# Performance work log

Measured on AMD Instinct MI355X. Metric: run time of the kernel, lower is better.

Reference implementation:

```python
import jax, jax.numpy as jnp
import numpy as np

B, S, H = 2, 2048, 1024
NUM_HEADS = 16
HEAD_DIM = H // NUM_HEADS  # 64
SCALE = HEAD_DIM ** -0.5


def apply_rope(x, cos, sin):
    # x: [B, nh, S, hd]; cos/sin: [1, 1, S, hd//2]
    x1 = x[..., ::2]
    x2 = x[..., 1::2]
    rotated = jnp.stack([x1 * cos - x2 * sin, x1 * sin + x2 * cos], axis=-1)
    return rotated.reshape(x.shape)


def setup_inputs() -> dict:
    key = jax.random.key(0)
    ks = jax.random.split(key, 7)
    return {
        "x": jax.random.normal(ks[0], (B, S, H), dtype=jnp.float32),
        "cos": jax.random.normal(ks[1], (S, HEAD_DIM // 2), dtype=jnp.float32),
        "sin": jax.random.normal(ks[2], (S, HEAD_DIM // 2), dtype=jnp.float32),
        "wq": jax.random.normal(ks[3], (H, H), dtype=jnp.float32) * (H ** -0.5),
        "wk": jax.random.normal(ks[4], (H, H), dtype=jnp.float32) * (H ** -0.5),
        "wv": jax.random.normal(ks[5], (H, H), dtype=jnp.float32) * (H ** -0.5),
        "wo": jax.random.normal(ks[6], (H, H), dtype=jnp.float32) * (H ** -0.5),
    }


def reference(x, cos, sin, wq, wk, wv, wo):
    b, s, h = x.shape
    nh, hd = NUM_HEADS, HEAD_DIM
    # torch Linear: y = x @ W.T
    q = (x @ wq.T).reshape(b, s, nh, hd).transpose(0, 2, 1, 3)  # [b, nh, s, hd]
    k = (x @ wk.T).reshape(b, s, nh, hd).transpose(0, 2, 1, 3)
    v = (x @ wv.T).reshape(b, s, nh, hd).transpose(0, 2, 1, 3)

    c = cos[None, None]  # [1,1,s,hd//2]
    sn = sin[None, None]
    q = apply_rope(q, c, sn)
    k = apply_rope(k, c, sn)

    scores = jnp.einsum("bhqd,bhkd->bhqk", q, k) * SCALE  # [b, nh, s, s]
    causal_mask = jnp.triu(jnp.ones((s, s), dtype=bool), k=1)
    scores = jnp.where(causal_mask[None, None], -jnp.inf, scores)
    attn = jax.nn.softmax(scores, axis=-1)
    out = jnp.einsum("bhqk,bhkd->bhqd", attn, v)  # [b, nh, s, hd]
    out = out.transpose(0, 2, 1, 3).reshape(b, s, h)
    return out @ wo.T
```

## Files before the change

### kernel.cpp

```cpp
#include <hip/hip_runtime.h>

typedef __attribute__((ext_vector_type(8))) __bf16 bf16x8;
typedef __attribute__((ext_vector_type(4))) float f32x4;
typedef __attribute__((ext_vector_type(4))) unsigned short ushort4v;

__device__ __forceinline__ unsigned short f2bf(float x) {
  union { float f; unsigned u; } v; v.f = x;
  unsigned r = v.u + 0x7fffu + ((v.u >> 16) & 1u);
  return (unsigned short)(r >> 16);
}

#define GLDS16(g, l) __builtin_amdgcn_global_load_lds( \
    (__attribute__((address_space(1))) void*)(g), \
    (__attribute__((address_space(3))) void*)(l), 16, 0, 0)

__global__ void cvt_f32_bf16(const float* __restrict__ src,
                             unsigned short* __restrict__ dst, int n4) {
  int i = blockIdx.x * blockDim.x + threadIdx.x;
  if (i >= n4) return;
  float4 v = reinterpret_cast<const float4*>(src)[i];
  ushort4v o;
  o.x = f2bf(v.x); o.y = f2bf(v.y); o.z = f2bf(v.z); o.w = f2bf(v.w);
  reinterpret_cast<ushort4v*>(dst)[i] = o;
}

template <int MODE>
__global__ __launch_bounds__(256) void gemm_bt(
    const unsigned short* __restrict__ A, const unsigned short* __restrict__ Bw,
    const float* __restrict__ cosT, const float* __restrict__ sinT,
    unsigned short* __restrict__ Qh, unsigned short* __restrict__ Kh,
    unsigned short* __restrict__ Vt, float* __restrict__ outF) {
  __shared__ __align__(16) unsigned char smA[2][8192];
  __shared__ __align__(16) unsigned char smB[2][8192];
  const int t = threadIdx.x;
  const int lane = t & 63, wvi = t >> 6;
  const int wr = wvi >> 1, wc = wvi & 1;
  const int g = lane >> 4, li = lane & 15;
  const int row0 = blockIdx.y * 128, col0 = blockIdx.x * 128;

  const int schunk = (t & 3) ^ ((t >> 2) & 3);
  const size_t arow = (size_t)(row0 + (t >> 2)) * 1024 + schunk * 8;
  const size_t brow = (size_t)(col0 + (t >> 2)) * 1024 + schunk * 8;

  f32x4 acc[4][4];
#pragma unroll
  for (int mi = 0; mi < 4; ++mi)
#pragma unroll
    for (int ni = 0; ni < 4; ++ni) acc[mi][ni] = (f32x4){0.f, 0.f, 0.f, 0.f};

  auto stage = [&](int buf, int k0) {
    GLDS16(A + arow + k0, &smA[buf][t * 16]);
    GLDS16(A + arow + 64 * 1024 + k0, &smA[buf][4096 + t * 16]);
    GLDS16(Bw + brow + k0, &smB[buf][t * 16]);
    GLDS16(Bw + brow + 64 * 1024 + k0, &smB[buf][4096 + t * 16]);
  };

  stage(0, 0);
  for (int kk = 0; kk < 32; ++kk) {
    __syncthreads();
    const int buf = kk & 1;
    if (kk < 31) stage(buf ^ 1, (kk + 1) * 32);
    bf16x8 af[4], bfr[4];
#pragma unroll
    for (int mi = 0; mi < 4; ++mi)
      af[mi] = *reinterpret_cast<const bf16x8*>(
          &smA[buf][((wr * 64 + mi * 16 + li) << 6) + ((g ^ (li & 3)) << 4)]);
#pragma unroll
    for (int ni = 0; ni < 4; ++ni)
      bfr[ni] = *reinterpret_cast<const bf16x8*>(
          &smB[buf][((wc * 64 + ni * 16 + li) << 6) + ((g ^ (li & 3)) << 4)]);
#pragma unroll
    for (int mi = 0; mi < 4; ++mi)
#pragma unroll
      for (int ni = 0; ni < 4; ++ni)
        acc[mi][ni] = __builtin_amdgcn_mfma_f32_16x16x32_bf16(
            af[mi], bfr[ni], acc[mi][ni], 0, 0, 0);
  }

#pragma unroll
  for (int mi = 0; mi < 4; ++mi) {
    const int rowb = row0 + wr * 64 + mi * 16 + g * 4;
#pragma unroll
    for (int ni = 0; ni < 4; ++ni) {
      const int col = col0 + wc * 64 + ni * 16 + li;
#pragma unroll
      for (int r = 0; r < 4; ++r) {
        float v = acc[mi][ni][r];
        const int rr = rowb + r;
        if (MODE == 1) {
          outF[(size_t)rr * 1024 + col] = v;
        } else {
          const int s = rr & 2047, b = rr >> 11;
          const int jj = col & 1023;
          const int h = jj >> 6, d = jj & 63;
          const int bh = b * 16 + h;
          const int typ = col >> 10;
          if (typ == 2) {
            Vt[((size_t)bh * 64 + d) * 2048 + s] = f2bf(v);
          } else {
            const float cs = cosT[s * 32 + (d >> 1)];
            const float sn = sinT[s * 32 + (d >> 1)];
            const float pr = __shfl_xor(v, 1);
            float rv = (d & 1) ? (pr * sn + v * cs) : (v * cs - pr * sn);
            if (typ == 0) rv *= 0.18033688011112042f;
            unsigned short* dst = (typ == 0) ? Qh : Kh;
            dst[((size_t)bh * 2048 + s) * 64 + d] = f2bf(rv);
          }
        }
      }
    }
  }
}

__global__ __launch_bounds__(512, 4) void attn_fwd(
    const unsigned short* __restrict__ Qh, const unsigned short* __restrict__ Kh,
    const unsigned short* __restrict__ Vt, unsigned short* __restrict__ Ob) {
  __shared__ __align__(16) unsigned short Plds[2][8][16][72];

  const int t = threadIdx.x, lane = t & 63, w = t >> 6;
  const int wg = w >> 2, wl = w & 3;
  const int g = lane >> 4, li = lane & 15;
  const int bh = blockIdx.x, y = blockIdx.y;
  const int qt = wg ? (31 - y) : y;
  const int q0 = qt * 64;

  const unsigned short* __restrict__ Kbh = Kh + (size_t)bh * 2048 * 64;
  const unsigned short* __restrict__ Vbh = Vt + (size_t)bh * 64 * 2048;

  bf16x8 qa[2];
  {
    const unsigned short* qrow =
        Qh + ((size_t)bh * 2048 + q0 + wl * 16 + li) * 64 + g * 8;
    qa[0] = *reinterpret_cast<const bf16x8*>(qrow);
    qa[1] = *reinterpret_cast<const bf16x8*>(qrow + 32);
  }

  float m_[4], l_[4];
  f32x4 oacc[4];
#pragma unroll
  for (int r = 0; r < 4; ++r) { m_[r] = -1e30f; l_[r] = 0.f; }
#pragma unroll
  for (int dt = 0; dt < 4; ++dt) oacc[dt] = (f32x4){0.f, 0.f, 0.f, 0.f};

  for (int kt = 0; kt <= qt; ++kt) {
    const int kv0 = kt * 64;
    const int par = kt & 1;

    f32x4 sacc[4];
#pragma unroll
    for (int ct = 0; ct < 4; ++ct) {
      const unsigned short* krow = Kbh + (size_t)(kv0 + ct * 16 + li) * 64 + g * 8;
      bf16x8 kb0 = *reinterpret_cast<const bf16x8*>(krow);
      bf16x8 kb1 = *reinterpret_cast<const bf16x8*>(krow + 32);
      f32x4 z = (f32x4){0.f, 0.f, 0.f, 0.f};
      z = __builtin_amdgcn_mfma_f32_16x16x32_bf16(qa[0], kb0, z, 0, 0, 0);
      z = __builtin_amdgcn_mfma_f32_16x16x32_bf16(qa[1], kb1, z, 0, 0, 0);
      sacc[ct] = z;
    }

    bf16x8 vb[8];
#pragma unroll
    for (int dt = 0; dt < 4; ++dt) {
      const unsigned short* vrow = Vbh + (size_t)(dt * 16 + li) * 2048 + kv0 + g * 8;
      vb[2 * dt] = *reinterpret_cast<const bf16x8*>(vrow);
      vb[2 * dt + 1] = *reinterpret_cast<const bf16x8*>(vrow + 32);
    }

    if (kt == qt) {
#pragma unroll
      for (int ct = 0; ct < 4; ++ct)
#pragma unroll
        for (int r = 0; r < 4; ++r)
          if (ct * 16 + li > wl * 16 + g * 4 + r) sacc[ct][r] = -1e30f;
    }

    float mnew[4], alpha[4];
#pragma unroll
    for (int r = 0; r < 4; ++r) {
      float tm = fmaxf(fmaxf(sacc[0][r], sacc[1][r]), fmaxf(sacc[2][r], sacc[3][r]));
      tm = fmaxf(tm, __shfl_xor(tm, 1));
      tm = fmaxf(tm, __shfl_xor(tm, 2));
      tm = fmaxf(tm, __shfl_xor(tm, 4));
      tm = fmaxf(tm, __shfl_xor(tm, 8));
      const float mn = fmaxf(m_[r], tm);
      mnew[r] = mn;
      alpha[r] = __builtin_amdgcn_exp2f(m_[r] - mn);
      m_[r] = mn;
    }
#pragma unroll
    for (int r = 0; r < 4; ++r) {
      float ps = 0.f;
#pragma unroll
      for (int ct = 0; ct < 4; ++ct) {
        const float p = __builtin_amdgcn_exp2f(sacc[ct][r] - mnew[r]);
        ps += p;
        Plds[par][w][g * 4 + r][ct * 16 + li] = f2bf(p);
      }
      l_[r] = l_[r] * alpha[r] + ps;
#pragma unroll
      for (int dt = 0; dt < 4; ++dt) oacc[dt][r] *= alpha[r];
    }
    __builtin_amdgcn_wave_barrier();
    bf16x8 pa0, pa1;
    __builtin_memcpy(&pa0, &Plds[par][w][li][g * 8], 16);
    __builtin_memcpy(&pa1, &Plds[par][w][li][32 + g * 8], 16);
    __builtin_amdgcn_sched_barrier(0);
#pragma unroll
    for (int dt = 0; dt < 4; ++dt) {
      oacc[dt] = __builtin_amdgcn_mfma_f32_16x16x32_bf16(pa0, vb[2 * dt], oacc[dt], 0, 0, 0);
      oacc[dt] = __builtin_amdgcn_mfma_f32_16x16x32_bf16(pa1, vb[2 * dt + 1], oacc[dt], 0, 0, 0);
    }
  }

  const int b = bh >> 4, h = bh & 15;
#pragma unroll
  for (int r = 0; r < 4; ++r) {
    float ls = l_[r];
    ls += __shfl_xor(ls, 1);
    ls += __shfl_xor(ls, 2);
    ls += __shfl_xor(ls, 4);
    ls += __shfl_xor(ls, 8);
    const float inv = 1.0f / ls;
    const int row = q0 + wl * 16 + g * 4 + r;
#pragma unroll
    for (int dt = 0; dt < 4; ++dt)
      Ob[((size_t)b * 2048 + row) * 1024 + h * 64 + dt * 16 + li] =
          f2bf(oacc[dt][r] * inv);
  }
}

extern "C" void kernel_launch(void* const* d_in, const int* in_sizes, int n_in,
                              void* d_out, int out_size, void* d_ws, size_t ws_size,
                              hipStream_t stream) {
  const float* x = (const float*)d_in[0];
  const float* cosT = (const float*)d_in[1];
  const float* sinT = (const float*)d_in[2];
  const float* wq = (const float*)d_in[3];
  const float* wk = (const float*)d_in[4];
  const float* wv = (const float*)d_in[5];
  const float* wo = (const float*)d_in[6];
  float* out = (float*)d_out;

  char* ws = (char*)d_ws;
  unsigned short* xb    = (unsigned short*)(ws);
  unsigned short* wqkvb = (unsigned short*)(ws + 8388608);
  unsigned short* wob   = (unsigned short*)(ws + 14680064);
  unsigned short* Qh    = (unsigned short*)(ws + 16777216);
  unsigned short* Kh    = (unsigned short*)(ws + 25165824);
  unsigned short* Vt    = (unsigned short*)(ws + 33554432);
  unsigned short* Ob    = (unsigned short*)(ws + 41943040);

  cvt_f32_bf16<<<4096, 256, 0, stream>>>(x, xb, 1048576);
  cvt_f32_bf16<<<1024, 256, 0, stream>>>(wq, wqkvb, 262144);
  cvt_f32_bf16<<<1024, 256, 0, stream>>>(wk, wqkvb + 1048576, 262144);
  cvt_f32_bf16<<<1024, 256, 0, stream>>>(wv, wqkvb + 2097152, 262144);
  cvt_f32_bf16<<<1024, 256, 0, stream>>>(wo, wob, 262144);

  gemm_bt<0><<<dim3(24, 32), 256, 0, stream>>>(xb, wqkvb, cosT, sinT, Qh, Kh, Vt,
                                               nullptr);
  attn_fwd<<<dim3(32, 16), 512, 0, stream>>>(Qh, Kh, Vt, Ob);
  gemm_bt<1><<<dim3(8, 32), 256, 0, stream>>>(Ob, wob, nullptr, nullptr, nullptr,
                                              nullptr, nullptr, out);
}
```

Measured before the change: 307.4 us.

## Prefetch next K tile into registers with double-buffered attention loop

Restructures the flash-attention inner loop into a manually double-buffered loop that loads the next K tile into registers while the current tile's QK^T and softmax run. It also switches to incrementing pointers and replaces the sched_barrier before the PV MFMAs with a masked one at the end of each step. The goal is to hide global load latency for K behind compute. The cost is extra register pressure from holding two K tiles, which could lower occupancy.

```diff
diff --git a/kernel.cpp b/kernel.cpp
--- a/kernel.cpp
+++ b/kernel.cpp
@@ -142,29 +142,42 @@
 #pragma unroll
   for (int dt = 0; dt < 4; ++dt) oacc[dt] = (f32x4){0.f, 0.f, 0.f, 0.f};
 
-  for (int kt = 0; kt <= qt; ++kt) {
-    const int kv0 = kt * 64;
-    const int par = kt & 1;
-
+  const unsigned short* kptr = Kbh + li * 64 + g * 8;
+  const unsigned short* vbase = Vbh + li * 2048 + g * 8;
+
+  bf16x8 k0[8], k1[8];
+#pragma unroll
+  for (int ct = 0; ct < 4; ++ct) {
+    k0[2 * ct] = *reinterpret_cast<const bf16x8*>(kptr + ct * 1024);
+    k0[2 * ct + 1] = *reinterpret_cast<const bf16x8*>(kptr + ct * 1024 + 32);
+  }
+
+  auto step = [&](bf16x8(&curK)[8], bf16x8(&nxtK)[8], int kt, int par) {
     f32x4 sacc[4];
 #pragma unroll
     for (int ct = 0; ct < 4; ++ct) {
-      const unsigned short* krow = Kbh + (size_t)(kv0 + ct * 16 + li) * 64 + g * 8;
-      bf16x8 kb0 = *reinterpret_cast<const bf16x8*>(krow);
-      bf16x8 kb1 = *reinterpret_cast<const bf16x8*>(krow + 32);
       f32x4 z = (f32x4){0.f, 0.f, 0.f, 0.f};
-      z = __builtin_amdgcn_mfma_f32_16x16x32_bf16(qa[0], kb0, z, 0, 0, 0);
-      z = __builtin_amdgcn_mfma_f32_16x16x32_bf16(qa[1], kb1, z, 0, 0, 0);
+      z = __builtin_amdgcn_mfma_f32_16x16x32_bf16(qa[0], curK[2 * ct], z, 0, 0, 0);
+      z = __builtin_amdgcn_mfma_f32_16x16x32_bf16(qa[1], curK[2 * ct + 1], z, 0, 0, 0);
       sacc[ct] = z;
     }
 
+    if (kt < qt) {
+      kptr += 4096;
+#pragma unroll
+      for (int ct = 0; ct < 4; ++ct) {
+        nxtK[2 * ct] = *reinterpret_cast<const bf16x8*>(kptr + ct * 1024);
+        nxtK[2 * ct + 1] = *reinterpret_cast<const bf16x8*>(kptr + ct * 1024 + 32);
+      }
+    }
+
     bf16x8 vb[8];
 #pragma unroll
     for (int dt = 0; dt < 4; ++dt) {
-      const unsigned short* vrow = Vbh + (size_t)(dt * 16 + li) * 2048 + kv0 + g * 8;
-      vb[2 * dt] = *reinterpret_cast<const bf16x8*>(vrow);
-      vb[2 * dt + 1] = *reinterpret_cast<const bf16x8*>(vrow + 32);
-    }
+      vb[2 * dt] = *reinterpret_cast<const bf16x8*>(vbase + dt * 32768);
+      vb[2 * dt + 1] = *reinterpret_cast<const bf16x8*>(vbase + dt * 32768 + 32);
+    }
+    vbase += 64;
 
     if (kt == qt) {
 #pragma unroll
@@ -204,12 +217,20 @@
     bf16x8 pa0, pa1;
     __builtin_memcpy(&pa0, &Plds[par][w][li][g * 8], 16);
     __builtin_memcpy(&pa1, &Plds[par][w][li][32 + g * 8], 16);
-    __builtin_amdgcn_sched_barrier(0);
 #pragma unroll
     for (int dt = 0; dt < 4; ++dt) {
       oacc[dt] = __builtin_amdgcn_mfma_f32_16x16x32_bf16(pa0, vb[2 * dt], oacc[dt], 0, 0, 0);
       oacc[dt] = __builtin_amdgcn_mfma_f32_16x16x32_bf16(pa1, vb[2 * dt + 1], oacc[dt], 0, 0, 0);
     }
+    __builtin_amdgcn_sched_barrier(0x38F);
+  };
+
+  int kt = 0;
+  while (true) {
+    step(k0, k1, kt, 0);
+    if (++kt > qt) break;
+    step(k1, k0, kt, 1);
+    if (++kt > qt) break;
   }
 
   const int b = bh >> 4, h = bh & 15;
```

Result: slower. 380.2 us (+23.7%).
